# Kernel optimization log

Hardware: AMD Instinct MI355X
Metric: run time of the kernel (lower is better)

The kernel has to match this reference:

```python
import jax, jax.numpy as jnp
import numpy as np

N_NODES = 100000
N_EDGES = 1600000
IN_DIM, HID_DIM, OUT_DIM = 2, 128, 128


def setup_inputs() -> dict:
    key = jax.random.key(0)
    ks = jax.random.split(key, 8)
    x = jax.random.normal(ks[0], (N_NODES, IN_DIM), dtype=jnp.float32)
    edge_index = jax.random.randint(ks[1], (2, N_EDGES), 0, N_NODES, dtype=jnp.int64)
    s = 0.1
    return {
        "x": x,
        "edge_index": edge_index,
        # SAGEConv layer 1: lin_l (on aggregated neighbors, with bias) + lin_r (root)
        "W_l1": jax.random.normal(ks[2], (IN_DIM, HID_DIM), dtype=jnp.float32) * s,
        "W_r1": jax.random.normal(ks[3], (IN_DIM, HID_DIM), dtype=jnp.float32) * s,
        "b1": jnp.zeros((HID_DIM,), dtype=jnp.float32),
        # SAGEConv layer 2
        "W_l2": jax.random.normal(ks[4], (HID_DIM, OUT_DIM), dtype=jnp.float32) * s,
        "W_r2": jax.random.normal(ks[5], (HID_DIM, OUT_DIM), dtype=jnp.float32) * s,
        "b2": jnp.zeros((OUT_DIM,), dtype=jnp.float32),
    }


def _sage_conv(h, src, dst, Wl, Wr, b):
    # PyG SAGEConv (aggr='mean'): out_i = Wl @ mean_{j in N(i)} h_j + Wr @ h_i + b
    msg = h[src]                                              # [E, D] gather
    agg = jax.ops.segment_sum(msg, dst, num_segments=N_NODES)  # [N, D] scatter-add
    deg = jax.ops.segment_sum(jnp.ones_like(dst, dtype=h.dtype), dst,
                              num_segments=N_NODES)
    agg = agg / jnp.maximum(deg, 1.0)[:, None]                # mean aggregation
    return agg @ Wl + h @ Wr + b


def reference(x, edge_index, W_l1, W_r1, b1, W_l2, W_r2, b2):
    src, dst = edge_index[0], edge_index[1]  # messages flow src -> dst
    h = _sage_conv(x, src, dst, W_l1, W_r1, b1)
    h = jax.nn.relu(h)  # dropout p=0.1 is identity in eval mode
    out = _sage_conv(h, src, dst, W_l2, W_r2, b2)
    return out
```

## Files before the change

### kernel.cpp

```cpp
#include <hip/hip_runtime.h>


using f32x4 = __attribute__((ext_vector_type(4))) float;
using f32x2 = __attribute__((ext_vector_type(2))) float;
using s16x8 = __attribute__((ext_vector_type(8))) short;

__device__ __forceinline__ unsigned short f32_to_bf16(float f) {
  unsigned int u = __float_as_uint(f);
  u += 0x7fffu + ((u >> 16) & 1u);
  return (unsigned short)(u >> 16);
}

#define EDGE_TILE 4096

__global__ __launch_bounds__(256) void k_bhist(const int* __restrict__ ei, int* __restrict__ bcnt,
                                               int E, int nb) {
  __shared__ int h[1024];
  int t = threadIdx.x;
  for (int i = t; i < nb; i += 256) h[i] = 0;
  __syncthreads();
  int tbeg = blockIdx.x * EDGE_TILE;
  int tend = min(tbeg + EDGE_TILE, E);
  const int* dstp = ei + E;
  for (int i = tbeg + t; i < tend; i += 256) atomicAdd(&h[dstp[i] >> 7], 1);
  __syncthreads();
  for (int i = t; i < nb; i += 256) if (h[i]) atomicAdd(&bcnt[i], h[i]);
}

__global__ __launch_bounds__(1024) void k_bscan(const int* __restrict__ bcnt, int* __restrict__ bbase,
                                                int* __restrict__ bcur, int nb, int E) {
  __shared__ int sm[2][1024];
  int t = threadIdx.x;
  int v0 = (t < nb) ? bcnt[t] : 0;
  sm[0][t] = v0;
  __syncthreads();
  int src = 0;
  for (int st = 1; st < 1024; st <<= 1) {
    int v = sm[src][t];
    if (t >= st) v += sm[src][t - st];
    sm[src ^ 1][t] = v; __syncthreads(); src ^= 1;
  }
  int ex = sm[src][t] - v0;
  if (t < nb) { bbase[t] = ex; bcur[t] = ex; }
  if (t == 0) bbase[nb] = E;
}

__global__ __launch_bounds__(256) void k_bscatter(const int* __restrict__ ei, int* __restrict__ bcur,
                                                  unsigned int* __restrict__ ebuf, int E, int nb) {
  __shared__ int h[1024];
  __shared__ int base[1024];
  int t = threadIdx.x;
  for (int i = t; i < nb; i += 256) h[i] = 0;
  __syncthreads();
  int tbeg = blockIdx.x * EDGE_TILE;
  int tend = min(tbeg + EDGE_TILE, E);
  const int* srcp = ei;
  const int* dstp = ei + E;
  for (int i = tbeg + t; i < tend; i += 256) atomicAdd(&h[dstp[i] >> 7], 1);
  __syncthreads();
  for (int i = t; i < nb; i += 256) {
    int c = h[i];
    base[i] = c ? atomicAdd(&bcur[i], c) : 0;
    h[i] = 0;
  }
  __syncthreads();
  for (int i = tbeg + t; i < tend; i += 256) {
    int d = dstp[i];
    int b = d >> 7;
    int r = atomicAdd(&h[b], 1);
    ebuf[base[b] + r] = ((unsigned)srcp[i] << 7) | (unsigned)(d & 127);
  }
}

__global__ __launch_bounds__(256) void k_bucket_csr(const unsigned int* __restrict__ ebuf,
                                                    const int* __restrict__ bbase,
                                                    int* __restrict__ offs, int* __restrict__ csr,
                                                    int N, int nb) {
  __shared__ int deg[128];
  __shared__ int loff[128];
  __shared__ int cur[128];
  int b = blockIdx.x;
  int t = threadIdx.x;
  int lo = bbase[b], hi = bbase[b + 1];
  if (t < 128) deg[t] = 0;
  __syncthreads();
  for (int i = lo + t; i < hi; i += 256) atomicAdd(&deg[ebuf[i] & 127], 1);
  __syncthreads();
  if (t < 128) loff[t] = deg[t];
  __syncthreads();
  for (int st = 1; st < 128; st <<= 1) {
    int v = 0;
    if (t < 128 && t >= st) v = loff[t - st];
    __syncthreads();
    if (t < 128) loff[t] += v;
    __syncthreads();
  }
  if (t < 128) {
    int ex = loff[t] - deg[t];
    cur[t] = ex;
    int node = b * 128 + t;
    if (node < N) offs[node] = lo + ex;
  }
  if (b == nb - 1 && t == 0) offs[N] = hi;
  __syncthreads();
  for (int i = lo + t; i < hi; i += 256) {
    unsigned int e = ebuf[i];
    int r = atomicAdd(&cur[e & 127], 1);
    csr[lo + r] = (int)(e >> 7);
  }
}

__global__ __launch_bounds__(256) void k_agg1(const int* __restrict__ offs, const int* __restrict__ csr,
                                              const float* __restrict__ x, float* __restrict__ agg1, int n) {
  int node = blockIdx.x * 256 + threadIdx.x;
  if (node >= n) return;
  int beg = offs[node], end = offs[node + 1];
  float s0 = 0.f, s1 = 0.f;
  const float2* x2 = (const float2*)x;
  for (int e = beg; e < end; ++e) {
    int s = csr[e];
    float2 v = x2[s];
    s0 += v.x; s1 += v.y;
  }
  agg1[2 * node] = s0; agg1[2 * node + 1] = s1;
}

__global__ __launch_bounds__(256) void k_layer1(const float* __restrict__ x, const float* __restrict__ agg1,
                                                const int* __restrict__ offs,
                                                const float* __restrict__ Wl, const float* __restrict__ Wr,
                                                const float* __restrict__ b1,
                                                unsigned int* __restrict__ h16,
                                                unsigned short* __restrict__ h8, int n) {
  int gid = blockIdx.x * 256 + threadIdx.x;
  int node = gid >> 6;
  if (node >= n) return;
  int c = (gid & 63) * 2;
  int deg = offs[node + 1] - offs[node];
  float sc = 1.0f / (float)max(deg, 1);
  float a0 = agg1[2 * node] * sc, a1 = agg1[2 * node + 1] * sc;
  float x0 = x[2 * node], x1 = x[2 * node + 1];
  float r0 = fmaf(a0, Wl[c],     fmaf(a1, Wl[128 + c],     fmaf(x0, Wr[c],     fmaf(x1, Wr[128 + c],     b1[c]))));
  float r1 = fmaf(a0, Wl[c + 1], fmaf(a1, Wl[128 + c + 1], fmaf(x0, Wr[c + 1], fmaf(x1, Wr[128 + c + 1], b1[c + 1]))));
  r0 = r0 > 0.f ? r0 : 0.f;
  r1 = r1 > 0.f ? r1 : 0.f;
  unsigned int packed = (unsigned int)f32_to_bf16(r0) | ((unsigned int)f32_to_bf16(r1) << 16);
  h16[(size_t)node * 64 + (gid & 63)] = packed;
  unsigned int p8 = (unsigned int)__builtin_amdgcn_cvt_pk_fp8_f32(r0, r1, 0, false);
  h8[(size_t)node * 64 + (gid & 63)] = (unsigned short)(p8 & 0xffffu);
}

__global__ __launch_bounds__(256) void k_prepw(const float* __restrict__ Wl2, const float* __restrict__ Wr2,
                                               unsigned short* __restrict__ wt) {
  int tid = blockIdx.x * 256 + threadIdx.x;
  if (tid >= 128 * 256) return;
  int c = tid >> 8, k = tid & 255;
  float v = (k < 128) ? Wl2[k * 128 + c] : Wr2[(k - 128) * 128 + c];
  wt[tid] = f32_to_bf16(v);
}

__global__ __launch_bounds__(256) void k_agg2(const int* __restrict__ offs, const int* __restrict__ csr,
                                              const unsigned char* __restrict__ h8,
                                              unsigned int* __restrict__ a16, int n) {
  int node = blockIdx.x * 4 + (threadIdx.x >> 6);
  if (node >= n) return;
  int lane = threadIdx.x & 63;
  int g  = lane >> 3;
  int cb = lane & 7;
  int beg = offs[node], end = offs[node + 1];
  float acc[16];
#pragma unroll
  for (int j = 0; j < 16; ++j) acc[j] = 0.f;
  for (int e = beg; e < end; e += 8) {
    int idx = e + g;
    int cidx = idx < end ? idx : end - 1;
    float w = idx < end ? 1.f : 0.f;
    int s = csr[cidx];
    uint4 v = *(const uint4*)(h8 + (size_t)s * 128 + cb * 16);
    f32x2 p;
    p = __builtin_amdgcn_cvt_pk_f32_fp8((int)v.x, false); acc[0] = fmaf(w, p[0], acc[0]);  acc[1] = fmaf(w, p[1], acc[1]);
    p = __builtin_amdgcn_cvt_pk_f32_fp8((int)v.x, true);  acc[2] = fmaf(w, p[0], acc[2]);  acc[3] = fmaf(w, p[1], acc[3]);
    p = __builtin_amdgcn_cvt_pk_f32_fp8((int)v.y, false); acc[4] = fmaf(w, p[0], acc[4]);  acc[5] = fmaf(w, p[1], acc[5]);
    p = __builtin_amdgcn_cvt_pk_f32_fp8((int)v.y, true);  acc[6] = fmaf(w, p[0], acc[6]);  acc[7] = fmaf(w, p[1], acc[7]);
    p = __builtin_amdgcn_cvt_pk_f32_fp8((int)v.z, false); acc[8] = fmaf(w, p[0], acc[8]);  acc[9] = fmaf(w, p[1], acc[9]);
    p = __builtin_amdgcn_cvt_pk_f32_fp8((int)v.z, true);  acc[10] = fmaf(w, p[0], acc[10]); acc[11] = fmaf(w, p[1], acc[11]);
    p = __builtin_amdgcn_cvt_pk_f32_fp8((int)v.w, false); acc[12] = fmaf(w, p[0], acc[12]); acc[13] = fmaf(w, p[1], acc[13]);
    p = __builtin_amdgcn_cvt_pk_f32_fp8((int)v.w, true);  acc[14] = fmaf(w, p[0], acc[14]); acc[15] = fmaf(w, p[1], acc[15]);
  }
#pragma unroll
  for (int j = 0; j < 16; ++j) {
    acc[j] += __shfl_xor(acc[j], 8, 64);
    acc[j] += __shfl_xor(acc[j], 16, 64);
    acc[j] += __shfl_xor(acc[j], 32, 64);
  }
  if (g == 0) {
    int deg = end - beg;
    float scale = 1.0f / (float)max(deg, 1);
    unsigned int u[8];
#pragma unroll
    for (int k = 0; k < 8; ++k)
      u[k] = (unsigned int)f32_to_bf16(acc[2 * k] * scale) |
             ((unsigned int)f32_to_bf16(acc[2 * k + 1] * scale) << 16);
    unsigned int* dst = a16 + (size_t)node * 64 + cb * 8;
    *(uint4*)dst       = make_uint4(u[0], u[1], u[2], u[3]);
    *(uint4*)(dst + 4) = make_uint4(u[4], u[5], u[6], u[7]);
  }
}

__global__ __launch_bounds__(256) void k_gemm(const unsigned short* __restrict__ a16,
                                              const unsigned short* __restrict__ h16,
                                              const unsigned short* __restrict__ wt,
                                              const float* __restrict__ b2,
                                              float* __restrict__ out, int nrows) {
  __shared__ unsigned short bs[64 * 264];
  int half = blockIdx.x & 1;
  int tg   = blockIdx.x >> 1;

#pragma unroll
  for (int i = 0; i < 8; ++i) {
    int c = threadIdx.x + i * 256;
    int row = c >> 5, off = c & 31;
    *(uint4*)(bs + row * 264 + off * 8) =
        *(const uint4*)(wt + ((size_t)(half * 64 + row)) * 256 + off * 8);
  }
  __syncthreads();

  int wv   = threadIdx.x >> 6;
  int lane = threadIdx.x & 63;
  int m16 = lane & 15, quad = lane >> 4;
  int tile = tg * 4 + wv;
  if (tile * 16 >= nrows) return;

  int r  = tile * 16 + m16;
  int rc = r < nrows ? r : nrows - 1;
  const unsigned short* arow = a16 + (size_t)rc * 128 + quad * 8;
  const unsigned short* hrow = h16 + (size_t)rc * 128 + quad * 8;

  s16x8 afrag[8];
#pragma unroll
  for (int c4 = 0; c4 < 4; ++c4) {
    afrag[c4]     = *(const s16x8*)(arow + c4 * 32);
    afrag[4 + c4] = *(const s16x8*)(hrow + c4 * 32);
  }

  f32x4 acc[4];
#pragma unroll
  for (int t = 0; t < 4; ++t) acc[t] = (f32x4){0.f, 0.f, 0.f, 0.f};

  const unsigned short* bbase = bs + m16 * 264 + quad * 8;
#pragma unroll
  for (int ch = 0; ch < 8; ++ch) {
#pragma unroll
    for (int t = 0; t < 4; ++t) {
      s16x8 bf = *(const s16x8*)(bbase + t * 16 * 264 + ch * 32);
      acc[t] = __builtin_amdgcn_mfma_f32_16x16x32_bf16(afrag[ch], bf, acc[t], 0, 0, 0);
    }
  }

#pragma unroll
  for (int t = 0; t < 4; ++t) {
    int col = half * 64 + t * 16 + m16;
    float bias = b2[col];
#pragma unroll
    for (int i = 0; i < 4; ++i) {
      int row = tile * 16 + quad * 4 + i;
      if (row < nrows) out[(size_t)row * 128 + col] = acc[t][i] + bias;
    }
  }
}

extern "C" void kernel_launch(void* const* d_in, const int* in_sizes, int n_in,
                              void* d_out, int out_size, void* d_ws, size_t ws_size,
                              hipStream_t stream) {
  const float* x    = (const float*)d_in[0];
  const int*   ei   = (const int*)d_in[1];
  const float* Wl1  = (const float*)d_in[2];
  const float* Wr1  = (const float*)d_in[3];
  const float* b1   = (const float*)d_in[4];
  const float* Wl2  = (const float*)d_in[5];
  const float* Wr2  = (const float*)d_in[6];
  const float* b2   = (const float*)d_in[7];
  float* out = (float*)d_out;

  const int N = in_sizes[0] / 2;
  const int E = in_sizes[1] / 2;
  const int nb = (N + 127) >> 7;

  char* p = (char*)d_ws;
  auto take = [&](size_t bytes) { char* r = p; p += (bytes + 255) & ~(size_t)255; return r; };
  int* bcnt            = (int*)take(1024 * 4);
  int* bbase           = (int*)take(1025 * 4);
  int* bcur            = (int*)take(1024 * 4);
  int* offs            = (int*)take((size_t)(N + 1) * 4);
  int* csr             = (int*)take((size_t)E * 4);
  unsigned int* ebuf   = (unsigned int*)take((size_t)E * 4);
  float* agg1          = (float*)take((size_t)N * 2 * 4);
  unsigned short* h16  = (unsigned short*)take((size_t)N * 128 * 2);
  unsigned short* a16  = (unsigned short*)take((size_t)N * 128 * 2);
  unsigned short* h8   = (unsigned short*)take((size_t)N * 128);
  unsigned short* wt   = (unsigned short*)take((size_t)128 * 256 * 2);

  const int nblk_e = (E + EDGE_TILE - 1) / EDGE_TILE;
  const int ntiles = (N + 15) / 16;

  hipMemsetAsync(bcnt, 0, 1024 * 4, stream);

  k_bhist     <<<nblk_e, 256, 0, stream>>>(ei, bcnt, E, nb);
  k_bscan     <<<1, 1024, 0, stream>>>(bcnt, bbase, bcur, nb, E);
  k_bscatter  <<<nblk_e, 256, 0, stream>>>(ei, bcur, ebuf, E, nb);
  k_bucket_csr<<<nb, 256, 0, stream>>>(ebuf, bbase, offs, csr, N, nb);
  k_agg1      <<<(N + 255) / 256, 256, 0, stream>>>(offs, csr, x, agg1, N);
  k_layer1    <<<((size_t)N * 64 + 255) / 256, 256, 0, stream>>>(x, agg1, offs, Wl1, Wr1, b1,
                                                                 (unsigned int*)h16, h8, N);
  k_prepw     <<<(128 * 256) / 256, 256, 0, stream>>>(Wl2, Wr2, wt);
  k_agg2      <<<(N + 3) / 4, 256, 0, stream>>>(offs, csr, (const unsigned char*)h8,
                                                (unsigned int*)a16, N);
  k_gemm      <<<((ntiles + 3) / 4) * 2, 256, 0, stream>>>(a16, h16, wt, b2, out, N);
}
```

Measured before the change: 274.3 us.

## Fuse layer-1 aggregation into CSR build and remap agg2 to 8 lanes per node

The layer-1 neighbor sum of x is now computed inside the bucket CSR kernel with shared-memory float atomics, so the separate agg1 kernel and its pass over csr are removed. The layer-2 aggregation now gives each node 8 lanes instead of a full wavefront, and each lane walks all of that node's edges two at a time, which removes the cross-group shuffle reduction and the masked padding iterations. The trade-offs are shared float atomic contention, a summation order that depends on scheduling, and per-lane serial loops whose length follows node degree. That can cause divergence within a wavefront.

```diff
diff --git a/kernel.cpp b/kernel.cpp
--- a/kernel.cpp
+++ b/kernel.cpp
@@ -74,17 +74,29 @@
 
 __global__ __launch_bounds__(256) void k_bucket_csr(const unsigned int* __restrict__ ebuf,
                                                     const int* __restrict__ bbase,
+                                                    const float* __restrict__ x,
                                                     int* __restrict__ offs, int* __restrict__ csr,
+                                                    float* __restrict__ agg1,
                                                     int N, int nb) {
   __shared__ int deg[128];
   __shared__ int loff[128];
   __shared__ int cur[128];
+  __shared__ float sx0[128];
+  __shared__ float sx1[128];
   int b = blockIdx.x;
   int t = threadIdx.x;
   int lo = bbase[b], hi = bbase[b + 1];
-  if (t < 128) deg[t] = 0;
-  __syncthreads();
-  for (int i = lo + t; i < hi; i += 256) atomicAdd(&deg[ebuf[i] & 127], 1);
+  if (t < 128) { deg[t] = 0; sx0[t] = 0.f; sx1[t] = 0.f; }
+  __syncthreads();
+  const float2* x2 = (const float2*)x;
+  for (int i = lo + t; i < hi; i += 256) {
+    unsigned int e = ebuf[i];
+    int d = e & 127;
+    float2 v = x2[e >> 7];
+    atomicAdd(&deg[d], 1);
+    atomicAdd(&sx0[d], v.x);
+    atomicAdd(&sx1[d], v.y);
+  }
   __syncthreads();
   if (t < 128) loff[t] = deg[t];
   __syncthreads();
@@ -99,7 +111,11 @@
     int ex = loff[t] - deg[t];
     cur[t] = ex;
     int node = b * 128 + t;
-    if (node < N) offs[node] = lo + ex;
+    if (node < N) {
+      offs[node] = lo + ex;
+      agg1[2 * node]     = sx0[t];
+      agg1[2 * node + 1] = sx1[t];
+    }
   }
   if (b == nb - 1 && t == 0) offs[N] = hi;
   __syncthreads();
@@ -108,21 +124,6 @@
     int r = atomicAdd(&cur[e & 127], 1);
     csr[lo + r] = (int)(e >> 7);
   }
-}
-
-__global__ __launch_bounds__(256) void k_agg1(const int* __restrict__ offs, const int* __restrict__ csr,
-                                              const float* __restrict__ x, float* __restrict__ agg1, int n) {
-  int node = blockIdx.x * 256 + threadIdx.x;
-  if (node >= n) return;
-  int beg = offs[node], end = offs[node + 1];
-  float s0 = 0.f, s1 = 0.f;
-  const float2* x2 = (const float2*)x;
-  for (int e = beg; e < end; ++e) {
-    int s = csr[e];
-    float2 v = x2[s];
-    s0 += v.x; s1 += v.y;
-  }
-  agg1[2 * node] = s0; agg1[2 * node + 1] = s1;
 }
 
 __global__ __launch_bounds__(256) void k_layer1(const float* __restrict__ x, const float* __restrict__ agg1,
@@ -158,52 +159,61 @@
   wt[tid] = f32_to_bf16(v);
 }
 
+#define ACC8(v)                                                                              \
+  do {                                                                                       \
+    f32x2 p;                                                                                 \
+    p = __builtin_amdgcn_cvt_pk_f32_fp8((int)(v).x, false); acc[0] += p[0];  acc[1] += p[1]; \
+    p = __builtin_amdgcn_cvt_pk_f32_fp8((int)(v).x, true);  acc[2] += p[0];  acc[3] += p[1]; \
+    p = __builtin_amdgcn_cvt_pk_f32_fp8((int)(v).y, false); acc[4] += p[0];  acc[5] += p[1]; \
+    p = __builtin_amdgcn_cvt_pk_f32_fp8((int)(v).y, true);  acc[6] += p[0];  acc[7] += p[1]; \
+    p = __builtin_amdgcn_cvt_pk_f32_fp8((int)(v).z, false); acc[8] += p[0];  acc[9] += p[1]; \
+    p = __builtin_amdgcn_cvt_pk_f32_fp8((int)(v).z, true);  acc[10] += p[0]; acc[11] += p[1];\
+    p = __builtin_amdgcn_cvt_pk_f32_fp8((int)(v).w, false); acc[12] += p[0]; acc[13] += p[1];\
+    p = __builtin_amdgcn_cvt_pk_f32_fp8((int)(v).w, true);  acc[14] += p[0]; acc[15] += p[1];\
+  } while (0)
+
 __global__ __launch_bounds__(256) void k_agg2(const int* __restrict__ offs, const int* __restrict__ csr,
                                               const unsigned char* __restrict__ h8,
                                               unsigned int* __restrict__ a16, int n) {
-  int node = blockIdx.x * 4 + (threadIdx.x >> 6);
+  int wv   = threadIdx.x >> 6;
+  int lane = threadIdx.x & 63;
+  int sub  = lane >> 3;
+  int cb   = lane & 7;
+  int node = blockIdx.x * 32 + wv * 8 + sub;
   if (node >= n) return;
-  int lane = threadIdx.x & 63;
-  int g  = lane >> 3;
-  int cb = lane & 7;
-  int beg = offs[node], end = offs[node + 1];
+  int beg = offs[node];
+  int end = offs[node + 1];
+  int deg = end - beg;
+  const unsigned char* hb = h8 + cb * 16;
+
   float acc[16];
 #pragma unroll
   for (int j = 0; j < 16; ++j) acc[j] = 0.f;
-  for (int e = beg; e < end; e += 8) {
-    int idx = e + g;
-    int cidx = idx < end ? idx : end - 1;
-    float w = idx < end ? 1.f : 0.f;
-    int s = csr[cidx];
-    uint4 v = *(const uint4*)(h8 + (size_t)s * 128 + cb * 16);
-    f32x2 p;
-    p = __builtin_amdgcn_cvt_pk_f32_fp8((int)v.x, false); acc[0] = fmaf(w, p[0], acc[0]);  acc[1] = fmaf(w, p[1], acc[1]);
-    p = __builtin_amdgcn_cvt_pk_f32_fp8((int)v.x, true);  acc[2] = fmaf(w, p[0], acc[2]);  acc[3] = fmaf(w, p[1], acc[3]);
-    p = __builtin_amdgcn_cvt_pk_f32_fp8((int)v.y, false); acc[4] = fmaf(w, p[0], acc[4]);  acc[5] = fmaf(w, p[1], acc[5]);
-    p = __builtin_amdgcn_cvt_pk_f32_fp8((int)v.y, true);  acc[6] = fmaf(w, p[0], acc[6]);  acc[7] = fmaf(w, p[1], acc[7]);
-    p = __builtin_amdgcn_cvt_pk_f32_fp8((int)v.z, false); acc[8] = fmaf(w, p[0], acc[8]);  acc[9] = fmaf(w, p[1], acc[9]);
-    p = __builtin_amdgcn_cvt_pk_f32_fp8((int)v.z, true);  acc[10] = fmaf(w, p[0], acc[10]); acc[11] = fmaf(w, p[1], acc[11]);
-    p = __builtin_amdgcn_cvt_pk_f32_fp8((int)v.w, false); acc[12] = fmaf(w, p[0], acc[12]); acc[13] = fmaf(w, p[1], acc[13]);
-    p = __builtin_amdgcn_cvt_pk_f32_fp8((int)v.w, true);  acc[14] = fmaf(w, p[0], acc[14]); acc[15] = fmaf(w, p[1], acc[15]);
-  }
-#pragma unroll
-  for (int j = 0; j < 16; ++j) {
-    acc[j] += __shfl_xor(acc[j], 8, 64);
-    acc[j] += __shfl_xor(acc[j], 16, 64);
-    acc[j] += __shfl_xor(acc[j], 32, 64);
-  }
-  if (g == 0) {
-    int deg = end - beg;
-    float scale = 1.0f / (float)max(deg, 1);
-    unsigned int u[8];
-#pragma unroll
-    for (int k = 0; k < 8; ++k)
-      u[k] = (unsigned int)f32_to_bf16(acc[2 * k] * scale) |
-             ((unsigned int)f32_to_bf16(acc[2 * k + 1] * scale) << 16);
-    unsigned int* dst = a16 + (size_t)node * 64 + cb * 8;
-    *(uint4*)dst       = make_uint4(u[0], u[1], u[2], u[3]);
-    *(uint4*)(dst + 4) = make_uint4(u[4], u[5], u[6], u[7]);
-  }
+
+  int t = 0;
+  for (; t + 1 < deg; t += 2) {
+    int s0 = csr[beg + t];
+    int s1 = csr[beg + t + 1];
+    uint4 v0 = *(const uint4*)(hb + (size_t)s0 * 128);
+    uint4 v1 = *(const uint4*)(hb + (size_t)s1 * 128);
+    ACC8(v0);
+    ACC8(v1);
+  }
+  if (t < deg) {
+    int s0 = csr[beg + t];
+    uint4 v0 = *(const uint4*)(hb + (size_t)s0 * 128);
+    ACC8(v0);
+  }
+
+  float scale = 1.0f / (float)max(deg, 1);
+  unsigned int u[8];
+#pragma unroll
+  for (int k = 0; k < 8; ++k)
+    u[k] = (unsigned int)f32_to_bf16(acc[2 * k] * scale) |
+           ((unsigned int)f32_to_bf16(acc[2 * k + 1] * scale) << 16);
+  unsigned int* dst = a16 + (size_t)node * 64 + cb * 8;
+  *(uint4*)dst       = make_uint4(u[0], u[1], u[2], u[3]);
+  *(uint4*)(dst + 4) = make_uint4(u[4], u[5], u[6], u[7]);
 }
 
 __global__ __launch_bounds__(256) void k_gemm(const unsigned short* __restrict__ a16,
@@ -307,12 +317,11 @@
   k_bhist     <<<nblk_e, 256, 0, stream>>>(ei, bcnt, E, nb);
   k_bscan     <<<1, 1024, 0, stream>>>(bcnt, bbase, bcur, nb, E);
   k_bscatter  <<<nblk_e, 256, 0, stream>>>(ei, bcur, ebuf, E, nb);
-  k_bucket_csr<<<nb, 256, 0, stream>>>(ebuf, bbase, offs, csr, N, nb);
-  k_agg1      <<<(N + 255) / 256, 256, 0, stream>>>(offs, csr, x, agg1, N);
+  k_bucket_csr<<<nb, 256, 0, stream>>>(ebuf, bbase, x, offs, csr, agg1, N, nb);
   k_layer1    <<<((size_t)N * 64 + 255) / 256, 256, 0, stream>>>(x, agg1, offs, Wl1, Wr1, b1,
                                                                  (unsigned int*)h16, h8, N);
   k_prepw     <<<(128 * 256) / 256, 256, 0, stream>>>(Wl2, Wr2, wt);
-  k_agg2      <<<(N + 3) / 4, 256, 0, stream>>>(offs, csr, (const unsigned char*)h8,
-                                                (unsigned int*)a16, N);
+  k_agg2      <<<(N + 31) / 32, 256, 0, stream>>>(offs, csr, (const unsigned char*)h8,
+                                                  (unsigned int*)a16, N);
   k_gemm      <<<((ntiles + 3) / 4) * 2, 256, 0, stream>>>(a16, h16, wt, b2, out, N);
 }
```

After: 252.7 us. 1.09x faster.
